# Performance work log

Measured on AMD Instinct MI355X. Metric: run time of the kernel, lower is better.

The kernel has to match this reference:

```python
import jax, jax.numpy as jnp
import numpy as np

N = 50000      # nodes
DEG = 16       # avg degree
E = N * DEG    # edges
FIN = 128
FQK = 64
FV = 64
H = 8


def setup_inputs() -> dict:
    key = jax.random.key(0)
    k1, k2, k3, k4 = jax.random.split(key, 4)
    x = jax.random.normal(k1, (N, FIN), dtype=jnp.float32)
    # torch Linear(Fin, 2*Fqk+Fv, bias=False); stored here as [Fin, Ftot] so y = x @ W
    W = jax.random.normal(k2, (FIN, 2 * FQK + FV), dtype=jnp.float32) / np.sqrt(FIN)
    # edges: src sorted and covering all nodes (required by scatter_softmax semantics)
    src = jnp.repeat(jnp.arange(N, dtype=jnp.int32), DEG)
    dest = jax.random.randint(k3, (E,), 0, N, dtype=jnp.int32)
    ei = jnp.stack([src, dest])  # [2, E]
    batch = jnp.sort(jax.random.randint(k4, (N,), 0, 64, dtype=jnp.int32))
    return {"x": x, "W": W, "batch": batch, "ei": ei}


def reference(x, W, batch, ei):
    n = x.shape[0]
    Fh = FQK // H   # per-head qk dim
    Fhv = FV // H   # per-head v dim
    scaling = float(Fh) ** (-0.5)

    qkv = x @ W  # [N, 2*Fqk+Fv]
    q, k, v = jnp.split(qkv, [FQK, 2 * FQK], axis=-1)
    q = (q * scaling).reshape(n, H, Fh)
    k = k.reshape(n, H, Fh)
    v = v.reshape(n, H, Fhv)

    src, dest = ei[0], ei[1]
    qs = q[src]   # [E, H, Fh]
    ks = k[dest]  # [E, H, Fh]
    vs = v[dest]  # [E, H, Fhv]

    aw = jnp.einsum("ehf,ehf->eh", qs, ks)  # per-edge per-head logits

    # segment softmax over src (numerically stable, same math as exp/segsum(exp))
    amax = jax.ops.segment_max(aw, src, num_segments=n)
    ex = jnp.exp(aw - amax[src])
    denom = jax.ops.segment_sum(ex, src, num_segments=n)
    aw = ex / denom[src]  # [E, H]

    out = jax.ops.segment_sum(aw[:, :, None] * vs, src, num_segments=n)  # [N, H, Fhv]
    return out.reshape(n, H * Fhv)
```

## Files before the change

kernel.cpp:

```cpp
#include <hip/hip_runtime.h>
#include <math.h>

#define N_NODES 50000
#define DEG 16
#define E_EDGES (N_NODES * DEG)
#define FIN 128
#define FTOT 192
#define FQK 64
#define FV 64
#define H 8

typedef __attribute__((ext_vector_type(8))) short short8;
typedef __attribute__((ext_vector_type(4))) float float4v;

__device__ inline unsigned short f2bf(float f) {
    unsigned int u = __float_as_uint(f);
    unsigned int r = u + 0x7fffu + ((u >> 16) & 1u);
    return (unsigned short)(r >> 16);
}
__device__ inline float bf2f(unsigned short b) {
    return __uint_as_float(((unsigned int)b) << 16);
}

__global__ void wt_prep(const float* __restrict__ W, unsigned short* __restrict__ Wt) {
    int t = blockIdx.x * 256 + threadIdx.x;
    if (t >= FIN * FTOT) return;
    int k = t / FTOT, n = t % FTOT;
    Wt[n * FIN + k] = f2bf(W[t]);
}

#define LDB 136
__global__ __launch_bounds__(256) void gemm_qkv(const float* __restrict__ x,
                                                const unsigned short* __restrict__ Wt,
                                                unsigned short* __restrict__ qkv) {
    __shared__ unsigned short Bt[FTOT * LDB];
    const int tid = threadIdx.x;

#pragma unroll
    for (int i = 0; i < 12; i++) {
        int c = tid + i * 256;
        int n = c >> 4, off = (c & 15) * 8;
        *(uint4*)(&Bt[n * LDB + off]) = *(const uint4*)(Wt + n * FIN + off);
    }

    const int wave = tid >> 6, lane = tid & 63;
    const int m = lane & 15, q = lane >> 4;
    const int row = blockIdx.x * 64 + wave * 16 + m;
    const int rowc = min(row, N_NODES - 1);

    short8 a[4];
    const float* xr = x + rowc * FIN;
#pragma unroll
    for (int s = 0; s < 4; s++) {
        float4v f0 = *(const float4v*)(xr + s * 32 + q * 8);
        float4v f1 = *(const float4v*)(xr + s * 32 + q * 8 + 4);
        short8 av;
        av[0] = (short)f2bf(f0.x); av[1] = (short)f2bf(f0.y);
        av[2] = (short)f2bf(f0.z); av[3] = (short)f2bf(f0.w);
        av[4] = (short)f2bf(f1.x); av[5] = (short)f2bf(f1.y);
        av[6] = (short)f2bf(f1.z); av[7] = (short)f2bf(f1.w);
        a[s] = av;
    }
    __syncthreads();

    const int drow0 = blockIdx.x * 64 + wave * 16 + q * 4;
#pragma unroll
    for (int ct = 0; ct < 12; ct++) {
        float4v acc = {0.f, 0.f, 0.f, 0.f};
#pragma unroll
        for (int s = 0; s < 4; s++) {
            short8 b = *(const short8*)(&Bt[(ct * 16 + m) * LDB + s * 32 + q * 8]);
            acc = __builtin_amdgcn_mfma_f32_16x16x32_bf16(a[s], b, acc, 0, 0, 0);
        }
        const int col = ct * 16 + m;
        int off; float scale;
        if (col < FQK)            { off = col;                    scale = 0.35355339059327373f; }
        else if (col < 2 * FQK)   { off = 64 + 2 * (col - 64);    scale = 1.f; }
        else                      { off = 64 + 2 * (col - 128) + 1; scale = 1.f; }
#pragma unroll
        for (int i = 0; i < 4; i++) {
            int r = drow0 + i;
            if (r < N_NODES) qkv[r * FTOT + off] = f2bf(acc[i] * scale);
        }
    }
}

__global__ __launch_bounds__(256) void attn(const unsigned short* __restrict__ qkv,
                                            const int* __restrict__ dest,
                                            float* __restrict__ out) {
    const int node = blockIdx.x * 4 + (threadIdx.x >> 6);
    const int lane = threadIdx.x & 63;
    if (node >= N_NODES) return;

    const float qv = bf2f(qkv[node * FTOT + lane]);
    const int dj = dest[node * DEG + (lane & 15)];

    unsigned int kv[DEG];
#pragma unroll
    for (int j = 0; j < DEG; j++) {
        const int d = __shfl(dj, j, 64);
        kv[j] = *(const unsigned int*)(qkv + d * FTOT + 64 + 2 * lane);
    }

    float lg[DEG];
#pragma unroll
    for (int j = 0; j < DEG; j++) {
        float kf = __uint_as_float(kv[j] << 16);
        float l = qv * kf;
        l += __shfl_xor(l, 1, 64);
        l += __shfl_xor(l, 2, 64);
        l += __shfl_xor(l, 4, 64);
        lg[j] = l;
    }
    float mx = lg[0];
#pragma unroll
    for (int j = 1; j < DEG; j++) mx = fmaxf(mx, lg[j]);
    float s = 0.f, o = 0.f;
#pragma unroll
    for (int j = 0; j < DEG; j++) {
        float p = __expf(lg[j] - mx);
        s += p;
        o = fmaf(p, __uint_as_float(kv[j] & 0xffff0000u), o);
    }
    out[node * 64 + lane] = o / s;
}

extern "C" void kernel_launch(void* const* d_in, const int* in_sizes, int n_in,
                              void* d_out, int out_size, void* d_ws, size_t ws_size,
                              hipStream_t stream) {
    const float* x = (const float*)d_in[0];
    const float* W = (const float*)d_in[1];
    const int* ei = (const int*)d_in[3];
    const int* dest = ei + E_EDGES;
    float* out = (float*)d_out;

    unsigned short* qkv = (unsigned short*)d_ws;
    unsigned short* Wt  = (unsigned short*)((char*)d_ws + 19200000);

    wt_prep<<<(FIN * FTOT + 255) / 256, 256, 0, stream>>>(W, Wt);
    gemm_qkv<<<(N_NODES + 63) / 64, 256, 0, stream>>>(x, Wt, qkv);
    attn<<<(N_NODES + 3) / 4, 256, 0, stream>>>(qkv, dest, out);
}
```

Before: 124.8 us.

## Stage GEMM output through LDS for coalesced stores; split edges across wave halves

The QKV GEMM now keeps all twelve accumulator tiles in registers, writes the bf16 results into shared memory (reusing the B-tile buffer), and then copies them out with coalesced 32-bit stores instead of scattered 16-bit stores. The attention kernel splits each wave into two halves that handle alternating edges. Each lane loads 8-byte K/V chunks covering two features, computes a partial online softmax over its half's edges, and merges the two halves with a cross-half max/rescale shuffle. This cuts per-edge load instructions and shuffle reductions, at the cost of more registers in the GEMM and extra reduction shuffles.

```diff
diff --git a/kernel.cpp b/kernel.cpp
--- a/kernel.cpp
+++ b/kernel.cpp
@@ -30,10 +30,12 @@
 }
 
 #define LDB 136
+#define LDC 194
 __global__ __launch_bounds__(256) void gemm_qkv(const float* __restrict__ x,
                                                 const unsigned short* __restrict__ Wt,
                                                 unsigned short* __restrict__ qkv) {
     __shared__ unsigned short Bt[FTOT * LDB];
+    unsigned short* Ct = Bt;
     const int tid = threadIdx.x;
 
 #pragma unroll
@@ -63,25 +65,41 @@
     }
     __syncthreads();
 
-    const int drow0 = blockIdx.x * 64 + wave * 16 + q * 4;
+    float4v acc[12];
+#pragma unroll
+    for (int ct = 0; ct < 12; ct++) acc[ct] = (float4v){0.f, 0.f, 0.f, 0.f};
 #pragma unroll
     for (int ct = 0; ct < 12; ct++) {
-        float4v acc = {0.f, 0.f, 0.f, 0.f};
 #pragma unroll
         for (int s = 0; s < 4; s++) {
             short8 b = *(const short8*)(&Bt[(ct * 16 + m) * LDB + s * 32 + q * 8]);
-            acc = __builtin_amdgcn_mfma_f32_16x16x32_bf16(a[s], b, acc, 0, 0, 0);
+            acc[ct] = __builtin_amdgcn_mfma_f32_16x16x32_bf16(a[s], b, acc[ct], 0, 0, 0);
         }
+    }
+    __syncthreads();
+
+    const int lrow0 = wave * 16 + q * 4;
+#pragma unroll
+    for (int ct = 0; ct < 12; ct++) {
         const int col = ct * 16 + m;
         int off; float scale;
-        if (col < FQK)            { off = col;                    scale = 0.35355339059327373f; }
-        else if (col < 2 * FQK)   { off = 64 + 2 * (col - 64);    scale = 1.f; }
-        else                      { off = 64 + 2 * (col - 128) + 1; scale = 1.f; }
+        if (col < FQK)          { off = col;                      scale = 0.35355339059327373f; }
+        else if (col < 2 * FQK) { off = 64 + 2 * (col - 64);      scale = 1.f; }
+        else                    { off = 64 + 2 * (col - 128) + 1; scale = 1.f; }
 #pragma unroll
-        for (int i = 0; i < 4; i++) {
-            int r = drow0 + i;
-            if (r < N_NODES) qkv[r * FTOT + off] = f2bf(acc[i] * scale);
-        }
+        for (int i = 0; i < 4; i++)
+            Ct[(lrow0 + i) * LDC + off] = f2bf(acc[ct][i] * scale);
+    }
+    __syncthreads();
+
+    unsigned int* qg = (unsigned int*)qkv;
+    const int base = blockIdx.x * 64;
+#pragma unroll
+    for (int i = 0; i < 24; i++) {
+        int l = tid + i * 256;
+        int r = l / 96, dw = l - r * 96;
+        if (base + r < N_NODES)
+            qg[(size_t)(base + r) * 96 + dw] = *(const unsigned int*)(&Ct[r * LDC + 2 * dw]);
     }
 }
 
@@ -90,39 +108,54 @@
                                             float* __restrict__ out) {
     const int node = blockIdx.x * 4 + (threadIdx.x >> 6);
     const int lane = threadIdx.x & 63;
+    const int half = lane >> 5;
+    const int l = lane & 31;
     if (node >= N_NODES) return;
 
-    const float qv = bf2f(qkv[node * FTOT + lane]);
+    const unsigned int qw = *(const unsigned int*)(qkv + node * FTOT + 2 * l);
+    const float q0 = bf2f((unsigned short)(qw & 0xffffu));
+    const float q1 = bf2f((unsigned short)(qw >> 16));
     const int dj = dest[node * DEG + (lane & 15)];
 
-    unsigned int kv[DEG];
+    uint2 kv[8];
 #pragma unroll
-    for (int j = 0; j < DEG; j++) {
-        const int d = __shfl(dj, j, 64);
-        kv[j] = *(const unsigned int*)(qkv + d * FTOT + 64 + 2 * lane);
+    for (int t = 0; t < 8; t++) {
+        const int d = __shfl(dj, 2 * t + half, 64);
+        kv[t] = *(const uint2*)(qkv + d * FTOT + 64 + 4 * l);
     }
 
-    float lg[DEG];
+    float lg[8];
 #pragma unroll
-    for (int j = 0; j < DEG; j++) {
-        float kf = __uint_as_float(kv[j] << 16);
-        float l = qv * kf;
-        l += __shfl_xor(l, 1, 64);
-        l += __shfl_xor(l, 2, 64);
-        l += __shfl_xor(l, 4, 64);
-        lg[j] = l;
+    for (int t = 0; t < 8; t++) {
+        const float k0 = bf2f((unsigned short)(kv[t].x & 0xffffu));
+        const float k1 = bf2f((unsigned short)(kv[t].y & 0xffffu));
+        float p = fmaf(q0, k0, q1 * k1);
+        p += __shfl_xor(p, 1, 64);
+        p += __shfl_xor(p, 2, 64);
+        lg[t] = p;
     }
     float mx = lg[0];
 #pragma unroll
-    for (int j = 1; j < DEG; j++) mx = fmaxf(mx, lg[j]);
-    float s = 0.f, o = 0.f;
+    for (int t = 1; t < 8; t++) mx = fmaxf(mx, lg[t]);
+    float s = 0.f, o0 = 0.f, o1 = 0.f;
 #pragma unroll
-    for (int j = 0; j < DEG; j++) {
-        float p = __expf(lg[j] - mx);
+    for (int t = 0; t < 8; t++) {
+        const float p = __expf(lg[t] - mx);
         s += p;
-        o = fmaf(p, __uint_as_float(kv[j] & 0xffff0000u), o);
+        o0 = fmaf(p, __uint_as_float(kv[t].x & 0xffff0000u), o0);
+        o1 = fmaf(p, __uint_as_float(kv[t].y & 0xffff0000u), o1);
     }
-    out[node * 64 + lane] = o / s;
+    const float mo = __shfl_xor(mx, 32, 64);
+    const float mn = fmaxf(mx, mo);
+    const float f = __expf(mx - mn);
+    s *= f; o0 *= f; o1 *= f;
+    s  += __shfl_xor(s, 32, 64);
+    o0 += __shfl_xor(o0, 32, 64);
+    o1 += __shfl_xor(o1, 32, 64);
+    if (half == 0) {
+        float2 r; r.x = o0 / s; r.y = o1 / s;
+        *(float2*)(out + node * 64 + 2 * l) = r;
+    }
 }
 
 extern "C" void kernel_launch(void* const* d_in, const int* in_sizes, int n_in,
```

Result: faster. 112.9 us (-9.5%).
